# Kernel tuning notes

Measured on AMD Instinct MI355X. Metric: run time of the kernel, lower is better.

The kernel has to match this reference:

```python
import jax, jax.numpy as jnp
import numpy as np

DIM_OUT = 64
ALPHA = 0.5


def setup_inputs() -> dict:
    key = jax.random.key(0)
    x = jax.random.uniform(key, (2000000, 1), dtype=jnp.float32)
    return {"x": x}


def reference(x) -> jnp.ndarray:
    # Gegenbauer polynomial recurrence, parallel over rows, sequential over order i.
    x_in = x.squeeze()                      # [n]
    c0 = jnp.ones_like(x_in)                # C_0 = 1
    c1 = 2.0 * ALPHA * x_in                 # C_1 = 2*alpha*x

    def step(carry, i):
        prev, prev2 = carry
        ci = ((2.0 * i - 2.0 + 2.0 * ALPHA) * x_in * prev
              + (-i + 2.0 - 2.0 * ALPHA) * prev2) / i
        return (ci, prev), ci

    orders = jnp.arange(2, DIM_OUT + 1, dtype=x_in.dtype)  # i = 2..dim_out
    _, cs = jax.lax.scan(step, (c1, c0), orders)           # [dim_out-1, n]
    # output is c[..., 1:] -> columns C_1..C_dim_out, shape [n, dim_out]
    out = jnp.concatenate([c1[None, :], cs], axis=0).T
    return out
```

## Files before the change

kernel.cpp:

```cpp
#include <hip/hip_runtime.h>

#define DIM_OUT 64
#define ALPHA 0.5f
#define BLOCK 256
#define CHUNK 32
#define LSTRIDE (CHUNK + 1)

__global__ __launch_bounds__(BLOCK) void geg_kernel(const float* __restrict__ x,
                                                    float* __restrict__ out,
                                                    int n) {
    __shared__ float lds[BLOCK * LSTRIDE];

    const int tid = threadIdx.x;
    const size_t base_row = (size_t)blockIdx.x * BLOCK;
    const size_t row = base_row + tid;

    const float xv = (row < (size_t)n) ? x[row] : 0.0f;

    float prev2 = 1.0f;
    float prev  = 2.0f * ALPHA * xv;

    float* myrow = lds + tid * LSTRIDE;

    myrow[0] = prev;
    #pragma unroll
    for (int i = 2; i <= CHUNK; ++i) {
        const float a   = (2.0f * (float)i - 2.0f + 2.0f * ALPHA);
        const float b   = (-(float)i + 2.0f - 2.0f * ALPHA);
        const float inv = 1.0f / (float)i;
        float ci = (a * xv * prev + b * prev2) * inv;
        prev2 = prev;
        prev  = ci;
        myrow[i - 1] = ci;
    }
    __syncthreads();

    #pragma unroll
    for (int j = 0; j < 8; ++j) {
        int f   = j * BLOCK + tid;
        int r   = f >> 3;
        int c4  = f & 7;
        size_t grow = base_row + r;
        if (grow < (size_t)n) {
            const float* w = lds + r * LSTRIDE + c4 * 4;
            float4 v = make_float4(w[0], w[1], w[2], w[3]);
            *(float4*)(out + grow * DIM_OUT + c4 * 4) = v;
        }
    }
    __syncthreads();

    #pragma unroll
    for (int i = CHUNK + 1; i <= DIM_OUT; ++i) {
        const float a   = (2.0f * (float)i - 2.0f + 2.0f * ALPHA);
        const float b   = (-(float)i + 2.0f - 2.0f * ALPHA);
        const float inv = 1.0f / (float)i;
        float ci = (a * xv * prev + b * prev2) * inv;
        prev2 = prev;
        prev  = ci;
        myrow[i - 1 - CHUNK] = ci;
    }
    __syncthreads();

    #pragma unroll
    for (int j = 0; j < 8; ++j) {
        int f   = j * BLOCK + tid;
        int r   = f >> 3;
        int c4  = f & 7;
        size_t grow = base_row + r;
        if (grow < (size_t)n) {
            const float* w = lds + r * LSTRIDE + c4 * 4;
            float4 v = make_float4(w[0], w[1], w[2], w[3]);
            *(float4*)(out + grow * DIM_OUT + CHUNK + c4 * 4) = v;
        }
    }
}

extern "C" void kernel_launch(void* const* d_in, const int* in_sizes, int n_in,
                              void* d_out, int out_size, void* d_ws, size_t ws_size,
                              hipStream_t stream) {
    const float* x = (const float*)d_in[0];
    float* out = (float*)d_out;
    int n = in_sizes[0];

    const int block = BLOCK;
    const int grid = (n + block - 1) / block;
    geg_kernel<<<grid, block, 0, stream>>>(x, out, n);
}
```

Measured before the change: 510.7 us.

## Shrink LDS staging chunks to 16 columns with XOR-swizzled float4 transpose

Splits the 64 output columns into four 16-column chunks staged through a smaller float4 LDS buffer instead of two 32-column chunks with a padded scalar layout. Writes and reads to LDS now use 128-bit accesses, and an XOR swizzle replaces padding to avoid bank conflicts. A launch-bounds occupancy hint of 8 blocks is added. The smaller LDS footprint is meant to raise occupancy for this write-bound kernel, at the cost of more barriers per block and narrower global store segments per row.

```diff
diff --git a/kernel.cpp b/kernel.cpp
--- a/kernel.cpp
+++ b/kernel.cpp
@@ -3,13 +3,13 @@
 #define DIM_OUT 64
 #define ALPHA 0.5f
 #define BLOCK 256
-#define CHUNK 32
-#define LSTRIDE (CHUNK + 1)
+#define CHUNK 16
+#define NF4 (CHUNK / 4)
 
-__global__ __launch_bounds__(BLOCK) void geg_kernel(const float* __restrict__ x,
-                                                    float* __restrict__ out,
-                                                    int n) {
-    __shared__ float lds[BLOCK * LSTRIDE];
+__global__ __launch_bounds__(BLOCK, 8) void geg_kernel(const float* __restrict__ x,
+                                                       float* __restrict__ out,
+                                                       int n) {
+    __shared__ float4 lds[BLOCK * NF4];
 
     const int tid = threadIdx.x;
     const size_t base_row = (size_t)blockIdx.x * BLOCK;
@@ -20,58 +20,46 @@
     float prev2 = 1.0f;
     float prev  = 2.0f * ALPHA * xv;
 
-    float* myrow = lds + tid * LSTRIDE;
-
-    myrow[0] = prev;
-    #pragma unroll
-    for (int i = 2; i <= CHUNK; ++i) {
-        const float a   = (2.0f * (float)i - 2.0f + 2.0f * ALPHA);
-        const float b   = (-(float)i + 2.0f - 2.0f * ALPHA);
-        const float inv = 1.0f / (float)i;
-        float ci = (a * xv * prev + b * prev2) * inv;
-        prev2 = prev;
-        prev  = ci;
-        myrow[i - 1] = ci;
-    }
-    __syncthreads();
+    const int wsw = (tid >> 1) & 3;
 
     #pragma unroll
-    for (int j = 0; j < 8; ++j) {
-        int f   = j * BLOCK + tid;
-        int r   = f >> 3;
-        int c4  = f & 7;
-        size_t grow = base_row + r;
-        if (grow < (size_t)n) {
-            const float* w = lds + r * LSTRIDE + c4 * 4;
-            float4 v = make_float4(w[0], w[1], w[2], w[3]);
-            *(float4*)(out + grow * DIM_OUT + c4 * 4) = v;
+    for (int chunk = 0; chunk < DIM_OUT / CHUNK; ++chunk) {
+        #pragma unroll
+        for (int s = 0; s < NF4; ++s) {
+            float v0, v1, v2, v3;
+            #pragma unroll
+            for (int k = 0; k < 4; ++k) {
+                const int ord = chunk * CHUNK + s * 4 + k + 1;
+                float ci;
+                if (ord == 1) {
+                    ci = prev;
+                } else {
+                    const float a   = (2.0f * (float)ord - 2.0f + 2.0f * ALPHA);
+                    const float b   = (-(float)ord + 2.0f - 2.0f * ALPHA);
+                    const float inv = 1.0f / (float)ord;
+                    ci = (a * xv * prev + b * prev2) * inv;
+                    prev2 = prev;
+                    prev  = ci;
+                }
+                if (k == 0) v0 = ci; else if (k == 1) v1 = ci;
+                else if (k == 2) v2 = ci; else v3 = ci;
+            }
+            lds[tid * NF4 + (s ^ wsw)] = make_float4(v0, v1, v2, v3);
         }
-    }
-    __syncthreads();
+        __syncthreads();
 
-    #pragma unroll
-    for (int i = CHUNK + 1; i <= DIM_OUT; ++i) {
-        const float a   = (2.0f * (float)i - 2.0f + 2.0f * ALPHA);
-        const float b   = (-(float)i + 2.0f - 2.0f * ALPHA);
-        const float inv = 1.0f / (float)i;
-        float ci = (a * xv * prev + b * prev2) * inv;
-        prev2 = prev;
-        prev  = ci;
-        myrow[i - 1 - CHUNK] = ci;
-    }
-    __syncthreads();
-
-    #pragma unroll
-    for (int j = 0; j < 8; ++j) {
-        int f   = j * BLOCK + tid;
-        int r   = f >> 3;
-        int c4  = f & 7;
-        size_t grow = base_row + r;
-        if (grow < (size_t)n) {
-            const float* w = lds + r * LSTRIDE + c4 * 4;
-            float4 v = make_float4(w[0], w[1], w[2], w[3]);
-            *(float4*)(out + grow * DIM_OUT + CHUNK + c4 * 4) = v;
+        #pragma unroll
+        for (int j = 0; j < 4; ++j) {
+            const int f  = j * BLOCK + tid;
+            const int r  = f >> 2;
+            const int c4 = f & 3;
+            const size_t grow = base_row + r;
+            if (grow < (size_t)n) {
+                float4 v = lds[r * NF4 + (c4 ^ ((r >> 1) & 3))];
+                *(float4*)(out + grow * DIM_OUT + chunk * CHUNK + c4 * 4) = v;
+            }
         }
+        __syncthreads();
     }
 }
 
@@ -82,7 +70,6 @@
     float* out = (float*)d_out;
     int n = in_sizes[0];
 
-    const int block = BLOCK;
-    const int grid = (n + block - 1) / block;
-    geg_kernel<<<grid, block, 0, stream>>>(x, out, n);
+    const int grid = (n + BLOCK - 1) / BLOCK;
+    geg_kernel<<<grid, BLOCK, 0, stream>>>(x, out, n);
 }
```

Result: slower. 586.9 us (+14.9%).
